# Kernel optimization log

Hardware: AMD Instinct MI355X
Metric: run time of the kernel (lower is better)

Reference implementation:

```python
import jax, jax.numpy as jnp
import numpy as np


def _proj(x_flat, w, b):
    # x_flat: (N, C, L), w: (O, C), b: (O,) -> (N, O, L)  (1x1x1 Conv3d)
    return jnp.einsum('oc,ncl->nol', w, x_flat) + b[None, :, None]


def setup_inputs() -> dict:
    key = jax.random.key(0)
    ks = jax.random.split(key, 9)
    C, Ch = 256, 128
    N, T, H, W = 2, 8, 28, 28
    s_in = 1.0 / np.sqrt(C)
    s_h = 1.0 / np.sqrt(Ch)
    return {
        'x': jax.random.normal(ks[0], (N, C, T, H, W), jnp.float32),
        'g_w': jax.random.normal(ks[1], (Ch, C), jnp.float32) * s_in,
        'g_b': jax.random.normal(ks[2], (Ch,), jnp.float32) * 0.01,
        'theta_w': jax.random.normal(ks[3], (Ch, C), jnp.float32) * s_in,
        'theta_b': jax.random.normal(ks[4], (Ch,), jnp.float32) * 0.01,
        'phi_w': jax.random.normal(ks[5], (Ch, C), jnp.float32) * s_in,
        'phi_b': jax.random.normal(ks[6], (Ch,), jnp.float32) * 0.01,
        'wz_w': jax.random.normal(ks[7], (C, Ch), jnp.float32) * s_h,
        'wz_b': jax.random.normal(ks[8], (C,), jnp.float32) * 0.01,
    }


def reference(x, g_w, g_b, theta_w, theta_b, phi_w, phi_b, wz_w, wz_b):
    N, C, T, H, W = x.shape
    L = T * H * W
    xf = x.reshape(N, C, L)                      # (N, C, L)
    g_x = _proj(xf, g_w, g_b)                    # (N, Ch, L)
    theta_x = _proj(xf, theta_w, theta_b)        # (N, Ch, L)
    phi_x = _proj(xf, phi_w, phi_b)              # (N, Ch, L)
    # f[n, i, j] = theta[n, :, i] . phi[n, :, j]
    f = jnp.einsum('nci,ncj->nij', theta_x, phi_x)  # (N, L, L)
    f = jax.nn.softmax(f, axis=-1)
    # y[n, c, i] = sum_j f[n, i, j] * g[n, c, j]
    y = jnp.einsum('nij,ncj->nci', f, g_x)          # (N, Ch, L)
    z = _proj(y, wz_w, wz_b)                        # (N, C, L)
    return z.reshape(N, C, T, H, W) + x
```

## Files before the change

kernel.cpp:

```cpp
#include <hip/hip_runtime.h>
#include <hip/hip_bf16.h>

constexpr int CIN    = 256;
constexpr int CH     = 128;
constexpr int LSEQ   = 6272;
constexpr int NBATCH = 2;
constexpr int NLCH   = NBATCH * LSEQ * CH;
constexpr float SHIFT = 40.0f;

typedef __attribute__((ext_vector_type(8))) __bf16 bf16x8;
typedef __attribute__((ext_vector_type(4))) float  f32x4;

__device__ __forceinline__ unsigned short f2bf(float f) {
    __hip_bfloat16 h = __float2bfloat16(f);
    return *reinterpret_cast<unsigned short*>(&h);
}
__device__ __forceinline__ float us2f(unsigned short h) {
    return __uint_as_float((unsigned)h << 16);
}

#define GLDS16(g, l) __builtin_amdgcn_global_load_lds(                      \
    (const __attribute__((address_space(1))) void*)(g),                     \
    (__attribute__((address_space(3))) void*)(l), 16, 0, 0)

__global__ __launch_bounds__(256) void prep_kernel(
    const float* __restrict__ th_w, const float* __restrict__ ph_w,
    const float* __restrict__ gw,   const float* __restrict__ wz_w,
    unsigned short* __restrict__ w3hi, unsigned short* __restrict__ w3lo,
    unsigned short* __restrict__ wzhi, unsigned short* __restrict__ wzlo)
{
    const int idx = blockIdx.x * 256 + threadIdx.x;
    if (idx < 98304) {
        float f = (idx < 32768) ? th_w[idx]
                : (idx < 65536) ? ph_w[idx - 32768] : gw[idx - 65536];
        unsigned short h = f2bf(f);
        w3hi[idx] = h;
        w3lo[idx] = f2bf(f - us2f(h));
    } else {
        const int j = idx - 98304;
        float f = wz_w[j];
        unsigned short h = f2bf(f);
        wzhi[j] = h;
        wzlo[j] = f2bf(f - us2f(h));
    }
}

__global__ __launch_bounds__(256) void proj_kernel(
    const float* __restrict__ x,
    const unsigned short* __restrict__ w3hi, const unsigned short* __restrict__ w3lo,
    const float* __restrict__ th_b, const float* __restrict__ ph_b,
    const float* __restrict__ gb,
    unsigned short* __restrict__ q, unsigned short* __restrict__ k,
    unsigned short* __restrict__ vt)
{
    constexpr int XS = 264;
    __shared__ unsigned short xhi[64][XS];
    __shared__ unsigned short xlo[64][XS];
    unsigned short (*gst)[137] = (unsigned short (*)[137])&xhi[0][0];

    const int t    = threadIdx.x;
    const int n    = blockIdx.y;
    const int l0   = blockIdx.x * 64;
    const int w    = t >> 6;
    const int lane = t & 63;
    const int lo   = lane & 15;
    const int quad = lane >> 4;

    {
        const int c = t;
        const float4* xr = (const float4*)(x + (size_t)(n * CIN + c) * LSEQ + l0);
        #pragma unroll
        for (int g4 = 0; g4 < 16; ++g4) {
            float4 v = xr[g4];
            float f[4] = { v.x, v.y, v.z, v.w };
            #pragma unroll
            for (int j = 0; j < 4; ++j) {
                unsigned short h = f2bf(f[j]);
                xhi[g4 * 4 + j][c] = h;
                xlo[g4 * 4 + j][c] = f2bf(f[j] - us2f(h));
            }
        }
    }

    float biasv[6];
    #pragma unroll
    for (int j = 0; j < 6; ++j) {
        int gch = 96 * w + 16 * j + lo;
        biasv[j] = (gch < 128) ? th_b[gch]
                 : (gch < 256) ? ph_b[gch - 128] : gb[gch - 256];
    }

    f32x4 acc[4][6];
    #pragma unroll
    for (int mt = 0; mt < 4; ++mt)
        #pragma unroll
        for (int j = 0; j < 6; ++j) acc[mt][j] = (f32x4){0.f, 0.f, 0.f, 0.f};

    __syncthreads();

    for (int ks = 0; ks < 8; ++ks) {
        const int k0 = ks * 32 + quad * 8;
        bf16x8 ahi[4], alo[4];
        #pragma unroll
        for (int mt = 0; mt < 4; ++mt) {
            ahi[mt] = *(const bf16x8*)&xhi[mt * 16 + lo][k0];
            alo[mt] = *(const bf16x8*)&xlo[mt * 16 + lo][k0];
        }
        #pragma unroll
        for (int j = 0; j < 6; ++j) {
            const size_t woff = (size_t)(96 * w + 16 * j + lo) * CIN + k0;
            bf16x8 bhi = *(const bf16x8*)(w3hi + woff);
            bf16x8 blo = *(const bf16x8*)(w3lo + woff);
            #pragma unroll
            for (int mt = 0; mt < 4; ++mt) {
                f32x4 a = acc[mt][j];
                a = __builtin_amdgcn_mfma_f32_16x16x32_bf16(ahi[mt], bhi, a, 0, 0, 0);
                a = __builtin_amdgcn_mfma_f32_16x16x32_bf16(alo[mt], bhi, a, 0, 0, 0);
                a = __builtin_amdgcn_mfma_f32_16x16x32_bf16(ahi[mt], blo, a, 0, 0, 0);
                acc[mt][j] = a;
            }
        }
    }

    __syncthreads();

    #pragma unroll
    for (int j = 0; j < 6; ++j) {
        const int base = 96 * w + 16 * j;
        #pragma unroll
        for (int mt = 0; mt < 4; ++mt) {
            #pragma unroll
            for (int r = 0; r < 4; ++r) {
                float val = acc[mt][j][r] + biasv[j];
                const int lrow = mt * 16 + quad * 4 + r;
                if (base < 256) {
                    unsigned short* dst = (base < 128) ? q : k;
                    const int ch = (base < 128) ? base + lo : base - 128 + lo;
                    dst[(size_t)(n * LSEQ + l0 + lrow) * CH + ch] = f2bf(val);
                } else {
                    gst[lrow][base - 256 + lo] = f2bf(val);
                }
            }
        }
    }
    __syncthreads();

    #pragma unroll
    for (int rep = 0; rep < 16; ++rep) {
        const int flat = rep * 256 + t;
        const int ch   = flat >> 5;
        const int lam  = flat & 31;
        unsigned u = (unsigned)gst[2 * lam][ch] | ((unsigned)gst[2 * lam + 1][ch] << 16);
        ((unsigned*)(vt + (size_t)(n * CH + ch) * LSEQ + l0))[lam] = u;
    }
}

__global__ __launch_bounds__(256, 2) void attn_kernel(
    const unsigned short* __restrict__ qb, const unsigned short* __restrict__ kb,
    const unsigned short* __restrict__ vtg,
    float* __restrict__ Op, float* __restrict__ lp,
    unsigned short* __restrict__ yb, int ns)
{
    constexpr int NTJ = LSEQ / 64;
    __shared__ unsigned short ks [2][64][128];
    __shared__ unsigned short vTs[2][128][64];
    __shared__ unsigned short ps [4][32][64];

    const int t    = threadIdx.x;
    const int s    = blockIdx.y;
    const int n    = blockIdx.z;
    const int i0   = blockIdx.x * 128;
    const int w    = t >> 6;
    const int lane = t & 63;
    const int lo   = lane & 15;
    const int quad = lane >> 4;
    const int lom  = (lo & 7) * 4;

    const int jt0 = (s * NTJ) / ns;
    const int jt1 = ((s + 1) * NTJ) / ns;

    const unsigned short* kbase = kb  + (size_t)n * LSEQ * CH;
    const unsigned short* vbase = vtg + (size_t)n * CH * LSEQ;

    bf16x8 qfrag[2][4];
    #pragma unroll
    for (int mt = 0; mt < 2; ++mt) {
        const unsigned short* qrow =
            qb + (size_t)(n * LSEQ + i0 + 32 * w + mt * 16 + lo) * CH;
        #pragma unroll
        for (int kc = 0; kc < 4; ++kc)
            qfrag[mt][kc] = *(const bf16x8*)(qrow + kc * 32 + quad * 8);
    }

    f32x4 o_acc[2][8];
    #pragma unroll
    for (int mt = 0; mt < 2; ++mt)
        #pragma unroll
        for (int nt = 0; nt < 8; ++nt) o_acc[mt][nt] = (f32x4){0.f, 0.f, 0.f, 0.f};
    float l_r[2][4] = {{0.f,0.f,0.f,0.f},{0.f,0.f,0.f,0.f}};

    auto stage = [&](int buf, int jt) {
        const int j0 = jt * 64;
        #pragma unroll
        for (int i = 0; i < 4; ++i) {
            const int c = w * 4 + i;
            {
                const int row = c * 4 + (lane >> 4);
                const int pcol = (lane & 15) * 4;
                const int lcol = pcol ^ ((row & 7) * 4);
                const unsigned short* g = kbase + (size_t)(j0 + row) * CH + lcol * 2;
                GLDS16(g, &ks[buf][0][0] + c * 512);
            }
            {
                const int row = c * 8 + (lane >> 3);
                const int pcol = (lane & 7) * 4;
                const int lcol = pcol ^ ((row & 7) * 4);
                const unsigned short* g = vbase + (size_t)row * LSEQ + j0 + lcol * 2;
                GLDS16(g, &vTs[buf][0][0] + c * 512);
            }
        }
    };

    int buf = 0;
    stage(0, jt0);
    __syncthreads();

    for (int jt = jt0; jt < jt1; ++jt) {
        if (jt + 1 < jt1) stage(buf ^ 1, jt + 1);

        f32x4 sacc[2][4];
        #pragma unroll
        for (int mt = 0; mt < 2; ++mt)
            #pragma unroll
            for (int ct = 0; ct < 4; ++ct) sacc[mt][ct] = (f32x4){0.f,0.f,0.f,0.f};
        #pragma unroll
        for (int ct = 0; ct < 4; ++ct) {
            #pragma unroll
            for (int kc = 0; kc < 4; ++kc) {
                const int pcol = (kc * 16 + quad * 4) ^ lom;
                bf16x8 b = *(const bf16x8*)&ks[buf][ct * 16 + lo][pcol * 2];
                #pragma unroll
                for (int mt = 0; mt < 2; ++mt)
                    sacc[mt][ct] = __builtin_amdgcn_mfma_f32_16x16x32_bf16(
                        qfrag[mt][kc], b, sacc[mt][ct], 0, 0, 0);
            }
        }

        __builtin_amdgcn_wave_barrier();
        #pragma unroll
        for (int mt = 0; mt < 2; ++mt) {
            #pragma unroll
            for (int ct = 0; ct < 4; ++ct) {
                #pragma unroll
                for (int r = 0; r < 4; ++r) {
                    float p = __expf(sacc[mt][ct][r] - SHIFT);
                    l_r[mt][r] += p;
                    const int row = mt * 16 + quad * 4 + r;
                    const int pdw = (ct * 8 + (lo >> 1)) ^ ((row & 7) * 4);
                    ps[w][row][pdw * 2 + (lo & 1)] = f2bf(p);
                }
            }
        }
        __builtin_amdgcn_wave_barrier();
        __builtin_amdgcn_s_waitcnt(0xC07F);

        bf16x8 pfrag[2][2];
        #pragma unroll
        for (int mt = 0; mt < 2; ++mt)
            #pragma unroll
            for (int kc = 0; kc < 2; ++kc) {
                const int pcol = (kc * 16 + quad * 4) ^ lom;
                pfrag[mt][kc] = *(const bf16x8*)&ps[w][mt * 16 + lo][pcol * 2];
            }

        #pragma unroll
        for (int nt = 0; nt < 8; ++nt) {
            #pragma unroll
            for (int kc = 0; kc < 2; ++kc) {
                const int pcol = (kc * 16 + quad * 4) ^ lom;
                bf16x8 b = *(const bf16x8*)&vTs[buf][nt * 16 + lo][pcol * 2];
                #pragma unroll
                for (int mt = 0; mt < 2; ++mt)
                    o_acc[mt][nt] = __builtin_amdgcn_mfma_f32_16x16x32_bf16(
                        pfrag[mt][kc], b, o_acc[mt][nt], 0, 0, 0);
            }
        }

        __syncthreads();
        buf ^= 1;
    }

    #pragma unroll
    for (int mt = 0; mt < 2; ++mt)
        #pragma unroll
        for (int r = 0; r < 4; ++r) {
            #pragma unroll
            for (int off = 1; off < 16; off <<= 1)
                l_r[mt][r] += __shfl_xor(l_r[mt][r], off);
        }

    if (Op != nullptr) {
        #pragma unroll
        for (int mt = 0; mt < 2; ++mt)
            #pragma unroll
            for (int r = 0; r < 4; ++r) {
                const int qi = i0 + 32 * w + mt * 16 + quad * 4 + r;
                float* orow = Op + ((size_t)(n * ns + s) * LSEQ + qi) * CH;
                #pragma unroll
                for (int nt = 0; nt < 8; ++nt)
                    orow[nt * 16 + lo] = o_acc[mt][nt][r];
                if (lo == 0)
                    lp[(size_t)(n * ns + s) * LSEQ + qi] = l_r[mt][r];
            }
    } else {
        #pragma unroll
        for (int mt = 0; mt < 2; ++mt)
            #pragma unroll
            for (int r = 0; r < 4; ++r) {
                const int qi = i0 + 32 * w + mt * 16 + quad * 4 + r;
                const float inv = 1.0f / l_r[mt][r];
                unsigned short* yr = yb + (size_t)(n * LSEQ + qi) * CH;
                #pragma unroll
                for (int nt = 0; nt < 8; ++nt)
                    yr[nt * 16 + lo] = f2bf(o_acc[mt][nt][r] * inv);
            }
    }
}

__global__ __launch_bounds__(256) void combine_kernel(
    const float* __restrict__ Op, const float* __restrict__ lp,
    unsigned short* __restrict__ yb, int ns)
{
    const int idx = blockIdx.x * 256 + threadIdx.x;
    const int n   = idx / (LSEQ * 32);
    const int rem = idx - n * (LSEQ * 32);
    const int l   = rem >> 5;
    const int c4  = (rem & 31) << 2;

    float4 o = make_float4(0.f, 0.f, 0.f, 0.f);
    float ls = 0.f;
    for (int s = 0; s < ns; ++s) {
        const float4 v = *(const float4*)&Op[((size_t)(n * ns + s) * LSEQ + l) * CH + c4];
        o.x += v.x; o.y += v.y; o.z += v.z; o.w += v.w;
        ls += lp[(size_t)(n * ns + s) * LSEQ + l];
    }
    const float inv = 1.0f / ls;
    unsigned r0 = (unsigned)f2bf(o.x * inv) | ((unsigned)f2bf(o.y * inv) << 16);
    unsigned r1 = (unsigned)f2bf(o.z * inv) | ((unsigned)f2bf(o.w * inv) << 16);
    uint2* dst = (uint2*)(yb + (size_t)(n * LSEQ + l) * CH + c4);
    *dst = make_uint2(r0, r1);
}

__global__ __launch_bounds__(256) void zout_kernel(
    const unsigned short* __restrict__ yb,
    const unsigned short* __restrict__ wzhi, const unsigned short* __restrict__ wzlo,
    const float* __restrict__ wz_b,
    const float* __restrict__ x, float* __restrict__ out)
{
    const int t    = threadIdx.x;
    const int n    = blockIdx.y;
    const int l0   = blockIdx.x * 64;
    const int w    = t >> 6;
    const int lane = t & 63;
    const int lo   = lane & 15;
    const int quad = lane >> 4;

    f32x4 acc[4][4];
    #pragma unroll
    for (int mt = 0; mt < 4; ++mt)
        #pragma unroll
        for (int nt = 0; nt < 4; ++nt) acc[mt][nt] = (f32x4){0.f, 0.f, 0.f, 0.f};

    const unsigned short* yrow[4];
    #pragma unroll
    for (int nt = 0; nt < 4; ++nt)
        yrow[nt] = yb + (size_t)(n * LSEQ + l0 + nt * 16 + lo) * CH;

    #pragma unroll
    for (int ks = 0; ks < 4; ++ks) {
        const int k0 = ks * 32 + quad * 8;
        bf16x8 bfr[4];
        #pragma unroll
        for (int nt = 0; nt < 4; ++nt)
            bfr[nt] = *(const bf16x8*)(yrow[nt] + k0);
        #pragma unroll
        for (int mt = 0; mt < 4; ++mt) {
            const size_t woff = (size_t)(64 * w + mt * 16 + lo) * CH + k0;
            bf16x8 ahi = *(const bf16x8*)(wzhi + woff);
            bf16x8 alo = *(const bf16x8*)(wzlo + woff);
            #pragma unroll
            for (int nt = 0; nt < 4; ++nt) {
                f32x4 a = acc[mt][nt];
                a = __builtin_amdgcn_mfma_f32_16x16x32_bf16(ahi, bfr[nt], a, 0, 0, 0);
                a = __builtin_amdgcn_mfma_f32_16x16x32_bf16(alo, bfr[nt], a, 0, 0, 0);
                acc[mt][nt] = a;
            }
        }
    }

    #pragma unroll
    for (int mt = 0; mt < 4; ++mt) {
        #pragma unroll
        for (int r = 0; r < 4; ++r) {
            const int c = 64 * w + mt * 16 + quad * 4 + r;
            const float bias = wz_b[c];
            const size_t base = (size_t)(n * CIN + c) * LSEQ + l0;
            #pragma unroll
            for (int nt = 0; nt < 4; ++nt) {
                const size_t off = base + nt * 16 + lo;
                out[off] = acc[mt][nt][r] + bias + x[off];
            }
        }
    }
}

extern "C" void kernel_launch(void* const* d_in, const int* in_sizes, int n_in,
                              void* d_out, int out_size, void* d_ws, size_t ws_size,
                              hipStream_t stream) {
    const float* x    = (const float*)d_in[0];
    const float* g_w  = (const float*)d_in[1];
    const float* g_b  = (const float*)d_in[2];
    const float* th_w = (const float*)d_in[3];
    const float* th_b = (const float*)d_in[4];
    const float* ph_w = (const float*)d_in[5];
    const float* ph_b = (const float*)d_in[6];
    const float* wz_w = (const float*)d_in[7];
    const float* wz_b = (const float*)d_in[8];
    float* out = (float*)d_out;

    unsigned short* q    = (unsigned short*)d_ws;
    unsigned short* k    = q + NLCH;
    unsigned short* vt   = k + NLCH;
    unsigned short* y    = vt + NLCH;
    unsigned short* w3hi = y + NLCH;
    unsigned short* w3lo = w3hi + 384 * 256;
    unsigned short* wzhi = w3lo + 384 * 256;
    unsigned short* wzlo = wzhi + 256 * 128;
    unsigned short* wend = wzlo + 256 * 128;

    const size_t base = (size_t)(wend - (unsigned short*)d_ws) * 2;
    const size_t per  = (size_t)NLCH * 4 + (size_t)NBATCH * LSEQ * 4;
    int ns = 0;
    if      (ws_size >= base + 4 * per) ns = 4;
    else if (ws_size >= base + 2 * per) ns = 2;
    else if (ws_size >= base + 1 * per) ns = 1;

    float* Op = (ns > 0) ? (float*)wend : nullptr;
    float* lp = (ns > 0) ? Op + (size_t)ns * NLCH : nullptr;

    prep_kernel<<<512, 256, 0, stream>>>(th_w, ph_w, g_w, wz_w,
                                         w3hi, w3lo, wzhi, wzlo);

    proj_kernel<<<dim3(LSEQ / 64, NBATCH), 256, 0, stream>>>(
        x, w3hi, w3lo, th_b, ph_b, g_b, q, k, vt);

    if (ns > 0) {
        attn_kernel<<<dim3(LSEQ / 128, ns, NBATCH), 256, 0, stream>>>(
            q, k, vt, Op, lp, y, ns);
        combine_kernel<<<(NBATCH * LSEQ * 32) / 256, 256, 0, stream>>>(Op, lp, y, ns);
    } else {
        attn_kernel<<<dim3(LSEQ / 128, 1, NBATCH), 256, 0, stream>>>(
            q, k, vt, nullptr, nullptr, y, 1);
    }

    zout_kernel<<<dim3(LSEQ / 64, NBATCH), 256, 0, stream>>>(
        y, wzhi, wzlo, wz_b, x, out);
}
```

Measured before the change: 192.0 us.

## Pre-transpose x to bf16 hi/lo, fuse split-K combine into output projection

The bf16 hi/lo split and transpose of x move into the prep kernel, so the projection kernel reads pre-transposed operands straight from global memory with no shared-memory staging. The projection and output kernels shrink their row tile from 64 to 32 to launch more blocks. The separate combine kernel is removed and the split-K reduction is folded into the output projection through shared memory, which saves one launch and the bf16 round-trip of y. The attention split count can now reach 5, at the cost of extra workspace and a larger intermediate transposed copy of x in memory.

```diff
diff --git a/kernel.cpp b/kernel.cpp
--- a/kernel.cpp
+++ b/kernel.cpp
@@ -6,6 +6,7 @@
 constexpr int LSEQ   = 6272;
 constexpr int NBATCH = 2;
 constexpr int NLCH   = NBATCH * LSEQ * CH;
+constexpr int NLC    = NBATCH * LSEQ * CIN;
 constexpr float SHIFT = 40.0f;
 
 typedef __attribute__((ext_vector_type(8))) __bf16 bf16x8;
@@ -24,64 +25,66 @@
     (__attribute__((address_space(3))) void*)(l), 16, 0, 0)
 
 __global__ __launch_bounds__(256) void prep_kernel(
+    const float* __restrict__ x,
     const float* __restrict__ th_w, const float* __restrict__ ph_w,
     const float* __restrict__ gw,   const float* __restrict__ wz_w,
     unsigned short* __restrict__ w3hi, unsigned short* __restrict__ w3lo,
-    unsigned short* __restrict__ wzhi, unsigned short* __restrict__ wzlo)
+    unsigned short* __restrict__ wzhi, unsigned short* __restrict__ wzlo,
+    unsigned short* __restrict__ xthi, unsigned short* __restrict__ xtlo)
 {
-    const int idx = blockIdx.x * 256 + threadIdx.x;
-    if (idx < 98304) {
-        float f = (idx < 32768) ? th_w[idx]
-                : (idx < 65536) ? ph_w[idx - 32768] : gw[idx - 65536];
-        unsigned short h = f2bf(f);
-        w3hi[idx] = h;
-        w3lo[idx] = f2bf(f - us2f(h));
+    const int b = blockIdx.x;
+    const int t = threadIdx.x;
+    if (b < 784) {
+        const int n  = b / 392;
+        const int l0 = (b % 392) * 16;
+        const int c  = t;
+        const float4* xr4 = (const float4*)(x + (size_t)(n * CIN + c) * LSEQ + l0);
+        float4 v[4] = { xr4[0], xr4[1], xr4[2], xr4[3] };
+        const float* f = (const float*)v;
+        unsigned short* bh = xthi + ((size_t)n * LSEQ + l0) * CIN + c;
+        unsigned short* bl = xtlo + ((size_t)n * LSEQ + l0) * CIN + c;
+        #pragma unroll
+        for (int j = 0; j < 16; ++j) {
+            unsigned short h = f2bf(f[j]);
+            bh[j * CIN] = h;
+            bl[j * CIN] = f2bf(f[j] - us2f(h));
+        }
     } else {
-        const int j = idx - 98304;
-        float f = wz_w[j];
-        unsigned short h = f2bf(f);
-        wzhi[j] = h;
-        wzlo[j] = f2bf(f - us2f(h));
+        const int idx = (b - 784) * 256 + t;
+        if (idx < 98304) {
+            float f = (idx < 32768) ? th_w[idx]
+                    : (idx < 65536) ? ph_w[idx - 32768] : gw[idx - 65536];
+            unsigned short h = f2bf(f);
+            w3hi[idx] = h;
+            w3lo[idx] = f2bf(f - us2f(h));
+        } else {
+            const int j = idx - 98304;
+            float f = wz_w[j];
+            unsigned short h = f2bf(f);
+            wzhi[j] = h;
+            wzlo[j] = f2bf(f - us2f(h));
+        }
     }
 }
 
 __global__ __launch_bounds__(256) void proj_kernel(
-    const float* __restrict__ x,
+    const unsigned short* __restrict__ xthi, const unsigned short* __restrict__ xtlo,
     const unsigned short* __restrict__ w3hi, const unsigned short* __restrict__ w3lo,
     const float* __restrict__ th_b, const float* __restrict__ ph_b,
     const float* __restrict__ gb,
     unsigned short* __restrict__ q, unsigned short* __restrict__ k,
     unsigned short* __restrict__ vt)
 {
-    constexpr int XS = 264;
-    __shared__ unsigned short xhi[64][XS];
-    __shared__ unsigned short xlo[64][XS];
-    unsigned short (*gst)[137] = (unsigned short (*)[137])&xhi[0][0];
+    __shared__ unsigned short gst[32][137];
 
     const int t    = threadIdx.x;
     const int n    = blockIdx.y;
-    const int l0   = blockIdx.x * 64;
+    const int l0   = blockIdx.x * 32;
     const int w    = t >> 6;
     const int lane = t & 63;
     const int lo   = lane & 15;
     const int quad = lane >> 4;
 
-    {
-        const int c = t;
-        const float4* xr = (const float4*)(x + (size_t)(n * CIN + c) * LSEQ + l0);
-        #pragma unroll
-        for (int g4 = 0; g4 < 16; ++g4) {
-            float4 v = xr[g4];
-            float f[4] = { v.x, v.y, v.z, v.w };
-            #pragma unroll
-            for (int j = 0; j < 4; ++j) {
-                unsigned short h = f2bf(f[j]);
-                xhi[g4 * 4 + j][c] = h;
-                xlo[g4 * 4 + j][c] = f2bf(f[j] - us2f(h));
-            }
-        }
-    }
-
     float biasv[6];
     #pragma unroll
     for (int j = 0; j < 6; ++j) {
@@ -90,21 +93,29 @@
                  : (gch < 256) ? ph_b[gch - 128] : gb[gch - 256];
     }
 
-    f32x4 acc[4][6];
-    #pragma unroll
-    for (int mt = 0; mt < 4; ++mt)
+    const unsigned short* ah[2];
+    const unsigned short* al[2];
+    #pragma unroll
+    for (int mt = 0; mt < 2; ++mt) {
+        const size_t row = (size_t)(n * LSEQ + l0 + mt * 16 + lo) * CIN;
+        ah[mt] = xthi + row;
+        al[mt] = xtlo + row;
+    }
+
+    f32x4 acc[2][6];
+    #pragma unroll
+    for (int mt = 0; mt < 2; ++mt)
         #pragma unroll
         for (int j = 0; j < 6; ++j) acc[mt][j] = (f32x4){0.f, 0.f, 0.f, 0.f};
 
-    __syncthreads();
-
+    #pragma unroll
     for (int ks = 0; ks < 8; ++ks) {
         const int k0 = ks * 32 + quad * 8;
-        bf16x8 ahi[4], alo[4];
-        #pragma unroll
-        for (int mt = 0; mt < 4; ++mt) {
-            ahi[mt] = *(const bf16x8*)&xhi[mt * 16 + lo][k0];
-            alo[mt] = *(const bf16x8*)&xlo[mt * 16 + lo][k0];
+        bf16x8 ahi[2], alo[2];
+        #pragma unroll
+        for (int mt = 0; mt < 2; ++mt) {
+            ahi[mt] = *(const bf16x8*)(ah[mt] + k0);
+            alo[mt] = *(const bf16x8*)(al[mt] + k0);
         }
         #pragma unroll
         for (int j = 0; j < 6; ++j) {
@@ -112,7 +123,7 @@
             bf16x8 bhi = *(const bf16x8*)(w3hi + woff);
             bf16x8 blo = *(const bf16x8*)(w3lo + woff);
             #pragma unroll
-            for (int mt = 0; mt < 4; ++mt) {
+            for (int mt = 0; mt < 2; ++mt) {
                 f32x4 a = acc[mt][j];
                 a = __builtin_amdgcn_mfma_f32_16x16x32_bf16(ahi[mt], bhi, a, 0, 0, 0);
                 a = __builtin_amdgcn_mfma_f32_16x16x32_bf16(alo[mt], bhi, a, 0, 0, 0);
@@ -122,13 +133,11 @@
         }
     }
 
-    __syncthreads();
-
     #pragma unroll
     for (int j = 0; j < 6; ++j) {
         const int base = 96 * w + 16 * j;
         #pragma unroll
-        for (int mt = 0; mt < 4; ++mt) {
+        for (int mt = 0; mt < 2; ++mt) {
             #pragma unroll
             for (int r = 0; r < 4; ++r) {
                 float val = acc[mt][j][r] + biasv[j];
@@ -146,10 +155,10 @@
     __syncthreads();
 
     #pragma unroll
-    for (int rep = 0; rep < 16; ++rep) {
+    for (int rep = 0; rep < 8; ++rep) {
         const int flat = rep * 256 + t;
-        const int ch   = flat >> 5;
-        const int lam  = flat & 31;
+        const int ch   = flat >> 4;
+        const int lam  = flat & 15;
         unsigned u = (unsigned)gst[2 * lam][ch] | ((unsigned)gst[2 * lam + 1][ch] << 16);
         ((unsigned*)(vt + (size_t)(n * CH + ch) * LSEQ + l0))[lam] = u;
     }
@@ -327,69 +336,80 @@
     }
 }
 
-__global__ __launch_bounds__(256) void combine_kernel(
+__global__ __launch_bounds__(256) void zout_kernel(
     const float* __restrict__ Op, const float* __restrict__ lp,
-    unsigned short* __restrict__ yb, int ns)
-{
-    const int idx = blockIdx.x * 256 + threadIdx.x;
-    const int n   = idx / (LSEQ * 32);
-    const int rem = idx - n * (LSEQ * 32);
-    const int l   = rem >> 5;
-    const int c4  = (rem & 31) << 2;
-
-    float4 o = make_float4(0.f, 0.f, 0.f, 0.f);
-    float ls = 0.f;
-    for (int s = 0; s < ns; ++s) {
-        const float4 v = *(const float4*)&Op[((size_t)(n * ns + s) * LSEQ + l) * CH + c4];
-        o.x += v.x; o.y += v.y; o.z += v.z; o.w += v.w;
-        ls += lp[(size_t)(n * ns + s) * LSEQ + l];
-    }
-    const float inv = 1.0f / ls;
-    unsigned r0 = (unsigned)f2bf(o.x * inv) | ((unsigned)f2bf(o.y * inv) << 16);
-    unsigned r1 = (unsigned)f2bf(o.z * inv) | ((unsigned)f2bf(o.w * inv) << 16);
-    uint2* dst = (uint2*)(yb + (size_t)(n * LSEQ + l) * CH + c4);
-    *dst = make_uint2(r0, r1);
-}
-
-__global__ __launch_bounds__(256) void zout_kernel(
     const unsigned short* __restrict__ yb,
     const unsigned short* __restrict__ wzhi, const unsigned short* __restrict__ wzlo,
     const float* __restrict__ wz_b,
-    const float* __restrict__ x, float* __restrict__ out)
+    const float* __restrict__ x, float* __restrict__ out, int ns)
 {
+    __shared__ unsigned short ysT[32][136];
+    __shared__ float linv[32];
+
     const int t    = threadIdx.x;
     const int n    = blockIdx.y;
-    const int l0   = blockIdx.x * 64;
+    const int l0   = blockIdx.x * 32;
     const int w    = t >> 6;
     const int lane = t & 63;
     const int lo   = lane & 15;
     const int quad = lane >> 4;
 
-    f32x4 acc[4][4];
+    if (ns > 0) {
+        if (t < 32) {
+            float ls = 0.f;
+            for (int s = 0; s < ns; ++s)
+                ls += lp[(size_t)(n * ns + s) * LSEQ + l0 + t];
+            linv[t] = 1.0f / ls;
+        }
+        __syncthreads();
+        #pragma unroll
+        for (int rep = 0; rep < 4; ++rep) {
+            const int flat = rep * 256 + t;
+            const int l  = flat >> 5;
+            const int c4 = (flat & 31) * 4;
+            float4 o = make_float4(0.f, 0.f, 0.f, 0.f);
+            for (int s = 0; s < ns; ++s) {
+                const float4 v = *(const float4*)
+                    &Op[((size_t)(n * ns + s) * LSEQ + l0 + l) * CH + c4];
+                o.x += v.x; o.y += v.y; o.z += v.z; o.w += v.w;
+            }
+            const float iv = linv[l];
+            unsigned r0 = (unsigned)f2bf(o.x * iv) | ((unsigned)f2bf(o.y * iv) << 16);
+            unsigned r1 = (unsigned)f2bf(o.z * iv) | ((unsigned)f2bf(o.w * iv) << 16);
+            *(uint2*)&ysT[l][c4] = make_uint2(r0, r1);
+        }
+    } else {
+        #pragma unroll
+        for (int rep = 0; rep < 4; ++rep) {
+            const int flat = rep * 256 + t;
+            const int l  = flat >> 5;
+            const int cu = flat & 31;
+            unsigned u = ((const unsigned*)(yb + (size_t)(n * LSEQ + l0 + l) * CH))[cu];
+            *(unsigned*)&ysT[l][cu * 2] = u;
+        }
+    }
+    __syncthreads();
+
+    f32x4 acc[4][2];
     #pragma unroll
     for (int mt = 0; mt < 4; ++mt)
         #pragma unroll
-        for (int nt = 0; nt < 4; ++nt) acc[mt][nt] = (f32x4){0.f, 0.f, 0.f, 0.f};
-
-    const unsigned short* yrow[4];
-    #pragma unroll
-    for (int nt = 0; nt < 4; ++nt)
-        yrow[nt] = yb + (size_t)(n * LSEQ + l0 + nt * 16 + lo) * CH;
+        for (int nt = 0; nt < 2; ++nt) acc[mt][nt] = (f32x4){0.f, 0.f, 0.f, 0.f};
 
     #pragma unroll
     for (int ks = 0; ks < 4; ++ks) {
         const int k0 = ks * 32 + quad * 8;
-        bf16x8 bfr[4];
-        #pragma unroll
-        for (int nt = 0; nt < 4; ++nt)
-            bfr[nt] = *(const bf16x8*)(yrow[nt] + k0);
+        bf16x8 bfr[2];
+        #pragma unroll
+        for (int nt = 0; nt < 2; ++nt)
+            bfr[nt] = *(const bf16x8*)&ysT[nt * 16 + lo][k0];
         #pragma unroll
         for (int mt = 0; mt < 4; ++mt) {
             const size_t woff = (size_t)(64 * w + mt * 16 + lo) * CH + k0;
             bf16x8 ahi = *(const bf16x8*)(wzhi + woff);
             bf16x8 alo = *(const bf16x8*)(wzlo + woff);
             #pragma unroll
-            for (int nt = 0; nt < 4; ++nt) {
+            for (int nt = 0; nt < 2; ++nt) {
                 f32x4 a = acc[mt][nt];
                 a = __builtin_amdgcn_mfma_f32_16x16x32_bf16(ahi, bfr[nt], a, 0, 0, 0);
                 a = __builtin_amdgcn_mfma_f32_16x16x32_bf16(alo, bfr[nt], a, 0, 0, 0);
@@ -406,7 +426,7 @@
             const float bias = wz_b[c];
             const size_t base = (size_t)(n * CIN + c) * LSEQ + l0;
             #pragma unroll
-            for (int nt = 0; nt < 4; ++nt) {
+            for (int nt = 0; nt < 2; ++nt) {
                 const size_t off = base + nt * 16 + lo;
                 out[off] = acc[mt][nt][r] + bias + x[off];
             }
@@ -436,33 +456,35 @@
     unsigned short* w3lo = w3hi + 384 * 256;
     unsigned short* wzhi = w3lo + 384 * 256;
     unsigned short* wzlo = wzhi + 256 * 128;
-    unsigned short* wend = wzlo + 256 * 128;
-
-    const size_t base = (size_t)(wend - (unsigned short*)d_ws) * 2;
+    unsigned short* xthi = wzlo + 256 * 128;
+    unsigned short* xtlo = xthi + NLC;
+    unsigned short* wend = xtlo + NLC;
+
+    const size_t base = (size_t)((char*)wend - (char*)d_ws);
     const size_t per  = (size_t)NLCH * 4 + (size_t)NBATCH * LSEQ * 4;
     int ns = 0;
-    if      (ws_size >= base + 4 * per) ns = 4;
+    if      (ws_size >= base + 5 * per) ns = 5;
+    else if (ws_size >= base + 4 * per) ns = 4;
     else if (ws_size >= base + 2 * per) ns = 2;
     else if (ws_size >= base + 1 * per) ns = 1;
 
     float* Op = (ns > 0) ? (float*)wend : nullptr;
     float* lp = (ns > 0) ? Op + (size_t)ns * NLCH : nullptr;
 
-    prep_kernel<<<512, 256, 0, stream>>>(th_w, ph_w, g_w, wz_w,
-                                         w3hi, w3lo, wzhi, wzlo);
-
-    proj_kernel<<<dim3(LSEQ / 64, NBATCH), 256, 0, stream>>>(
-        x, w3hi, w3lo, th_b, ph_b, g_b, q, k, vt);
+    prep_kernel<<<1296, 256, 0, stream>>>(x, th_w, ph_w, g_w, wz_w,
+                                          w3hi, w3lo, wzhi, wzlo, xthi, xtlo);
+
+    proj_kernel<<<dim3(LSEQ / 32, NBATCH), 256, 0, stream>>>(
+        xthi, xtlo, w3hi, w3lo, th_b, ph_b, g_b, q, k, vt);
 
     if (ns > 0) {
         attn_kernel<<<dim3(LSEQ / 128, ns, NBATCH), 256, 0, stream>>>(
             q, k, vt, Op, lp, y, ns);
-        combine_kernel<<<(NBATCH * LSEQ * 32) / 256, 256, 0, stream>>>(Op, lp, y, ns);
     } else {
         attn_kernel<<<dim3(LSEQ / 128, 1, NBATCH), 256, 0, stream>>>(
             q, k, vt, nullptr, nullptr, y, 1);
     }
 
-    zout_kernel<<<dim3(LSEQ / 64, NBATCH), 256, 0, stream>>>(
-        y, wzhi, wzlo, wz_b, x, out);
-}
+    zout_kernel<<<dim3(LSEQ / 32, NBATCH), 256, 0, stream>>>(
+        Op, lp, y, wzhi, wzlo, wz_b, x, out, ns);
+}
```

Result: no change. 194.0 us (+1.1%).
